# Kernel optimization log

Measured on AMD Instinct MI355X. Metric: run time of the kernel, lower is better.

Reference implementation:

```python
import jax, jax.numpy as jnp
import numpy as np

NUM_HEADS = 12
C_HEAD_DIM = 4   # int(1/dim_ratio)
S_HEAD_DIM = 16  # head_dim * dim_ratio
HEAD_DIM = C_HEAD_DIM * S_HEAD_DIM  # 64


def setup_inputs() -> dict:
    key = jax.random.key(0)
    ks = jax.random.split(key, 5)
    B, N, C, D = 8, 196, 12, 768
    x = jax.random.normal(ks[0], (B, N, C, D), dtype=jnp.float32)
    w_qkv_c = jax.random.normal(ks[1], (NUM_HEADS * 3 * C_HEAD_DIM, D), dtype=jnp.float32) * 0.02
    w_qkv_s = jax.random.normal(ks[2], (NUM_HEADS * 3 * S_HEAD_DIM, D), dtype=jnp.float32) * 0.02
    w_proj = jax.random.normal(ks[3], (D, D), dtype=jnp.float32) * 0.02
    b_proj = jnp.zeros((D,), dtype=jnp.float32)
    return {"x": x, "w_qkv_c": w_qkv_c, "w_qkv_s": w_qkv_s, "w_proj": w_proj, "b_proj": b_proj}


def _sdpa(q, k, v):
    # PyTorch F.scaled_dot_product_attention default scale: 1/sqrt(q.shape[-1])
    scale = q.shape[-1] ** -0.5
    attn = jax.nn.softmax(jnp.einsum('...qd,...kd->...qk', q * scale, k), axis=-1)
    return jnp.einsum('...qk,...kd->...qd', attn, v)


def reference(x, w_qkv_c, w_qkv_s, w_proj, b_proj):
    B, N, C, D = x.shape
    H, chd, shd = NUM_HEADS, C_HEAD_DIM, S_HEAD_DIM
    # channel-attention qkv: (3, B, H, N, C, chd)
    qkv_c = (x @ w_qkv_c.T).reshape(B, N, C, 3, H, chd).transpose(3, 0, 4, 1, 2, 5)
    qc, kc, vc = qkv_c[0], qkv_c[1], qkv_c[2]
    # spatial-attention qkv: (3, B, H, N, C, shd) -> attend over N
    qkv_s = (x @ w_qkv_s.T).reshape(B, N, C, 3, H, shd).transpose(3, 0, 4, 1, 2, 5)
    qs, ks, vs = qkv_s[0], qkv_s[1], qkv_s[2]
    qs, ks, vs = (t.swapaxes(-2, -3) for t in (qs, ks, vs))  # (B,H,C,N,shd)
    # spatial attention over N, then back to (B,H,N,C,shd)
    xs = _sdpa(qs, ks, vs).swapaxes(-2, -3)
    # channel attention over C: (B,H,N,C,chd)
    xc = _sdpa(qc, kc, vc)
    # outer product combine: (B,H,N,C,chd,shd) -> (B,H,N,C,head_dim)
    out = (xc[..., :, None] * xs[..., None, :]).reshape(B, H, N, C, chd * shd)
    # (B,N,H,C,hd) -> reshape (B,N,C,D) (row-major, matches torch)
    out = out.swapaxes(1, 2).reshape(B, N, C, D)
    return out @ w_proj.T + b_proj
```

## Files before the change

### kernel.cpp

```cpp
#include <hip/hip_runtime.h>
#include <math.h>

#define B_  8
#define N_  196
#define C_  12
#define D_  768
#define H_  12
#define R_  (B_*N_*C_)
#define KDIM 768
#define NQKV_PAD 768

typedef _Float16 f16x8 __attribute__((ext_vector_type(8)));
typedef _Float16 f16x4 __attribute__((ext_vector_type(4)));
typedef __fp16 fp16x2 __attribute__((ext_vector_type(2)));
typedef __attribute__((ext_vector_type(4))) float f32x4;

__device__ inline unsigned short f2h(float f) {
    union { _Float16 h; unsigned short u; } v; v.h = (_Float16)f; return v.u;
}
__device__ inline float h2f(unsigned short u) {
    union { unsigned short u; _Float16 h; } v; v.u = u; return (float)v.h;
}
__device__ inline unsigned pk2u(float a, float b) {
    union { fp16x2 h; unsigned u; } v;
    v.h = __builtin_amdgcn_cvt_pkrtz(a, b);
    return v.u;
}
__device__ inline unsigned scale2(unsigned u, float s) {
    return pk2u(h2f((unsigned short)(u & 0xffff)) * s,
                h2f((unsigned short)(u >> 16)) * s);
}

__global__ __launch_bounds__(256) void convert_weights(
    const float* __restrict__ wc, const float* __restrict__ ws,
    const float* __restrict__ wp,
    unsigned short* __restrict__ wqkv_h, unsigned short* __restrict__ wp_h)
{
    int i = (blockIdx.x * 256 + threadIdx.x) * 4;
    float4 v; unsigned short* dh; int off;
    if (i < 768 * 768) {
        off = i;
        const int r = off / 768, k = off % 768;
        v = make_float4(0.f, 0.f, 0.f, 0.f);
        if (r < 144)      v = *reinterpret_cast<const float4*>(wc + r * 768 + k);
        else if (r < 720) v = *reinterpret_cast<const float4*>(ws + (r - 144) * 768 + k);
        dh = wqkv_h;
    } else {
        off = i - 768 * 768;
        if (off >= 768 * 768) return;
        v = *reinterpret_cast<const float4*>(wp + off);
        dh = wp_h;
    }
    uint2 h;
    h.x = pk2u(v.x, v.y);
    h.y = pk2u(v.z, v.w);
    *reinterpret_cast<uint2*>(dh + off) = h;
}

#define BM 128
#define BN 128
#define BK 64

__device__ inline void gload16(const unsigned short* src, void* ldsbase) {
    __builtin_amdgcn_global_load_lds(
        (const __attribute__((address_space(1))) unsigned int*)src,
        (__attribute__((address_space(3))) unsigned int*)ldsbase, 16, 0, 0);
}

__global__ __launch_bounds__(512, 2) void gemm_qkv_fused(
    const float* __restrict__ Af, const unsigned short* __restrict__ Bh,
    unsigned short* __restrict__ outh, int M, int Nt, int K, int ntiles)
{
    __shared__ unsigned short sA[2][BM][BK];
    __shared__ unsigned short sB[2][BN][BK];

    const int nwg = gridDim.x;
    const int bid = blockIdx.x;
    const int xcd = bid & 7, slot = bid >> 3;
    const int q = nwg >> 3, r = nwg & 7;
    const int wg = (xcd < r ? xcd * (q + 1) : r * (q + 1) + (xcd - r) * q) + slot;
    const int mt = wg / ntiles, nt = wg - mt * ntiles;
    const int m0 = mt * BM, n0 = nt * BN;

    const int tid = threadIdx.x;
    const int w = tid >> 6, l = tid & 63;
    const int fl = l & 15, g = l >> 4;
    const int wr = (w >> 2) * 64;
    const int wc = (w & 3) * 32;

    f32x4 acc[4][2];
    #pragma unroll
    for (int i = 0; i < 4; ++i)
        #pragma unroll
        for (int j = 0; j < 2; ++j)
            acc[i][j] = (f32x4){0.f, 0.f, 0.f, 0.f};

    const int srow = w * 16 + (l >> 3);
    const int scol = ((l & 7) ^ (l >> 3)) * 8;

    float4 a0, a1, a2, a3;

#define LOADA(kk) {                                                                         \
    const float* paf = Af + (size_t)(m0 + srow) * K + (kk) + scol;                          \
    a0 = *reinterpret_cast<const float4*>(paf);                                             \
    a1 = *reinterpret_cast<const float4*>(paf + 4);                                         \
    a2 = *reinterpret_cast<const float4*>(paf + 8 * K);                                     \
    a3 = *reinterpret_cast<const float4*>(paf + 8 * K + 4); }

#define WRITEA(buf) {                                                                       \
    char* da = (char*)sA + (buf) * 16384 + w * 2048 + l * 16;                               \
    uint4 v0 = { pk2u(a0.x,a0.y), pk2u(a0.z,a0.w), pk2u(a1.x,a1.y), pk2u(a1.z,a1.w) };      \
    uint4 v1 = { pk2u(a2.x,a2.y), pk2u(a2.z,a2.w), pk2u(a3.x,a3.y), pk2u(a3.z,a3.w) };      \
    *reinterpret_cast<uint4*>(da) = v0;                                                     \
    *reinterpret_cast<uint4*>(da + 1024) = v1; }

#define STAGEB(buf, kk) {                                                                   \
    const unsigned short* pb = Bh + (size_t)(n0 + srow) * K + (kk) + scol;                  \
    char* db = (char*)sB + (buf) * 16384 + w * 2048;                                        \
    gload16(pb,          db);                                                               \
    gload16(pb + 8 * K,  db + 1024); }

    LOADA(0);
    STAGEB(0, 0);
    asm volatile("s_waitcnt vmcnt(2)" ::: "memory");
    WRITEA(0);
    LOADA(BK);
    asm volatile("s_waitcnt lgkmcnt(0)" ::: "memory");

    const int KT = K / BK;
    int cur = 0;
    for (int t = 0; t < KT; ++t) {
        if (t + 1 < KT) {
            STAGEB(cur ^ 1, (t + 1) * BK);
            asm volatile("s_waitcnt vmcnt(2)" ::: "memory");
        } else {
            asm volatile("s_waitcnt vmcnt(0)" ::: "memory");
        }
        asm volatile("s_barrier" ::: "memory");

        {
            const int rcol = (g ^ (fl & 7)) * 8;
            f16x8 ah[4];
            #pragma unroll
            for (int fm = 0; fm < 4; ++fm)
                ah[fm] = *reinterpret_cast<const f16x8*>(&sA[cur][wr + fm * 16 + fl][rcol]);
            __builtin_amdgcn_s_setprio(1);
            #pragma unroll
            for (int fn = 0; fn < 2; ++fn) {
                const f16x8 bf = *reinterpret_cast<const f16x8*>(&sB[cur][wc + fn * 16 + fl][rcol]);
                #pragma unroll
                for (int fm = 0; fm < 4; ++fm)
                    acc[fm][fn] = __builtin_amdgcn_mfma_f32_16x16x32_f16(ah[fm], bf, acc[fm][fn], 0, 0, 0);
            }
            __builtin_amdgcn_s_setprio(0);
        }
        if (t + 1 < KT) WRITEA(cur ^ 1);
        if (t + 2 < KT) LOADA((t + 2) * BK);
        {
            const int rcol = ((4 + g) ^ (fl & 7)) * 8;
            f16x8 ah[4];
            #pragma unroll
            for (int fm = 0; fm < 4; ++fm)
                ah[fm] = *reinterpret_cast<const f16x8*>(&sA[cur][wr + fm * 16 + fl][rcol]);
            __builtin_amdgcn_s_setprio(1);
            #pragma unroll
            for (int fn = 0; fn < 2; ++fn) {
                const f16x8 bf = *reinterpret_cast<const f16x8*>(&sB[cur][wc + fn * 16 + fl][rcol]);
                #pragma unroll
                for (int fm = 0; fm < 4; ++fm)
                    acc[fm][fn] = __builtin_amdgcn_mfma_f32_16x16x32_f16(ah[fm], bf, acc[fm][fn], 0, 0, 0);
            }
            __builtin_amdgcn_s_setprio(0);
        }
        asm volatile("s_waitcnt lgkmcnt(0)" ::: "memory");
        asm volatile("s_barrier" ::: "memory");
        cur ^= 1;
    }
#undef LOADA
#undef WRITEA
#undef STAGEB

    const int rg = g * 4;
    #pragma unroll
    for (int fm = 0; fm < 4; ++fm)
        #pragma unroll
        for (int fn = 0; fn < 2; ++fn) {
            const int row = m0 + wr + fm * 16 + rg;
            const int col = n0 + wc + fn * 16 + fl;
            #pragma unroll
            for (int rr = 0; rr < 4; ++rr)
                outh[(size_t)(row + rr) * Nt + col] = f2h(acc[fm][fn][rr]);
        }
}

__global__ __launch_bounds__(512, 2) void gemm_f16(
    const unsigned short* __restrict__ Ah, const unsigned short* __restrict__ Bh,
    const float* __restrict__ bias,
    float* __restrict__ outp, int M, int Nt, int K, int ntiles)
{
    __shared__ unsigned short sA[2][BM][BK];
    __shared__ unsigned short sB[2][BN][BK];

    const int nwg = gridDim.x;
    const int bid = blockIdx.x;
    const int xcd = bid & 7, slot = bid >> 3;
    const int q = nwg >> 3, r = nwg & 7;
    const int wg = (xcd < r ? xcd * (q + 1) : r * (q + 1) + (xcd - r) * q) + slot;
    const int mt = wg / ntiles, nt = wg - mt * ntiles;
    const int m0 = mt * BM, n0 = nt * BN;

    const int tid = threadIdx.x;
    const int w = tid >> 6, l = tid & 63;
    const int fl = l & 15, g = l >> 4;
    const int wr = (w >> 2) * 64;
    const int wc = (w & 3) * 32;

    f32x4 acc[4][2];
    #pragma unroll
    for (int i = 0; i < 4; ++i)
        #pragma unroll
        for (int j = 0; j < 2; ++j)
            acc[i][j] = (f32x4){0.f, 0.f, 0.f, 0.f};

    const int srow = w * 16 + (l >> 3);
    const int scol = ((l & 7) ^ (l >> 3)) * 8;

#define STAGE(buf, kk) {                                                                    \
    const unsigned short* pa = Ah + (size_t)(m0 + srow) * K + (kk) + scol;                  \
    const unsigned short* pb = Bh + (size_t)(n0 + srow) * K + (kk) + scol;                  \
    char* da = (char*)sA + (buf) * 16384 + w * 2048;                                        \
    char* db = (char*)sB + (buf) * 16384 + w * 2048;                                        \
    gload16(pa,          da);                                                               \
    gload16(pa + 8 * K,  da + 1024);                                                        \
    gload16(pb,          db);                                                               \
    gload16(pb + 8 * K,  db + 1024); }

    STAGE(0, 0);

    const int KT = K / BK;
    int cur = 0;
    for (int t = 0; t < KT; ++t) {
        if (t + 1 < KT) {
            STAGE(cur ^ 1, (t + 1) * BK);
            asm volatile("s_waitcnt vmcnt(4)" ::: "memory");
        } else {
            asm volatile("s_waitcnt vmcnt(0)" ::: "memory");
        }
        asm volatile("s_barrier" ::: "memory");

        #pragma unroll
        for (int ks = 0; ks < 2; ++ks) {
            const int rcol = ((ks * 4 + g) ^ (fl & 7)) * 8;
            f16x8 ah[4];
            #pragma unroll
            for (int fm = 0; fm < 4; ++fm)
                ah[fm] = *reinterpret_cast<const f16x8*>(&sA[cur][wr + fm * 16 + fl][rcol]);
            __builtin_amdgcn_s_setprio(1);
            #pragma unroll
            for (int fn = 0; fn < 2; ++fn) {
                const f16x8 bf = *reinterpret_cast<const f16x8*>(&sB[cur][wc + fn * 16 + fl][rcol]);
                #pragma unroll
                for (int fm = 0; fm < 4; ++fm)
                    acc[fm][fn] = __builtin_amdgcn_mfma_f32_16x16x32_f16(ah[fm], bf, acc[fm][fn], 0, 0, 0);
            }
            __builtin_amdgcn_s_setprio(0);
        }
        asm volatile("s_barrier" ::: "memory");
        cur ^= 1;
    }
#undef STAGE

    const int rg = g * 4;
    #pragma unroll
    for (int fm = 0; fm < 4; ++fm)
        #pragma unroll
        for (int fn = 0; fn < 2; ++fn) {
            const int row = m0 + wr + fm * 16 + rg;
            const int col = n0 + wc + fn * 16 + fl;
            const float bv = bias[col];
            #pragma unroll
            for (int rr = 0; rr < 4; ++rr)
                outp[(size_t)(row + rr) * Nt + col] = acc[fm][fn][rr] + bv;
        }
}

__global__ __launch_bounds__(256) void spatial_attn_mfma(
    const unsigned short* __restrict__ qkv,
    unsigned short* __restrict__ xs_out)
{
    __shared__ unsigned short Kl[224][24];
    __shared__ unsigned short Ql[208][24];
    __shared__ unsigned short Vt[16][236];

    const int bid2 = blockIdx.x;
    const int half = bid2 & 1;
    const int bid = bid2 >> 1;
    const int c = bid % 12;
    const int h = (bid / 12) % 12;
    const int b = bid / 144;
    const int tid = threadIdx.x;
    const int w = tid >> 6, l = tid & 63;
    const int fl = l & 15, g = l >> 4;
    const int qbase = half * 7;
    const int ntl = 7 - half;

    const float qs = 0.25f * 1.4426950408889634f;
    for (int idx = tid; idx < N_ * 2; idx += 256) {
        const int n = idx >> 1, eh = (idx & 1) * 8;
        const unsigned short* base =
            qkv + (size_t)((b * N_ + n) * 12 + c) * NQKV_PAD + 144 + h * 16 + eh;
        const uint4 q4 = *reinterpret_cast<const uint4*>(base);
        const uint4 k4 = *reinterpret_cast<const uint4*>(base + 192);
        const uint4 v4 = *reinterpret_cast<const uint4*>(base + 384);
        uint4 qsc;
        qsc.x = scale2(q4.x, qs); qsc.y = scale2(q4.y, qs);
        qsc.z = scale2(q4.z, qs); qsc.w = scale2(q4.w, qs);
        *reinterpret_cast<uint4*>(&Ql[n][eh]) = qsc;
        *reinterpret_cast<uint4*>(&Kl[n][eh]) = k4;
        Vt[eh + 0][n] = (unsigned short)(v4.x & 0xffff);
        Vt[eh + 1][n] = (unsigned short)(v4.x >> 16);
        Vt[eh + 2][n] = (unsigned short)(v4.y & 0xffff);
        Vt[eh + 3][n] = (unsigned short)(v4.y >> 16);
        Vt[eh + 4][n] = (unsigned short)(v4.z & 0xffff);
        Vt[eh + 5][n] = (unsigned short)(v4.z >> 16);
        Vt[eh + 6][n] = (unsigned short)(v4.w & 0xffff);
        Vt[eh + 7][n] = (unsigned short)(v4.w >> 16);
    }
    for (int idx = tid; idx < 16 * 28; idx += 256) {
        const int d = idx / 28, n = 196 + idx % 28;
        Vt[d][n] = 0;
    }
    __syncthreads();

    f32x4 accO[2];
    float lsum[2];
    #pragma unroll
    for (int j = 0; j < 2; ++j) {
        accO[j] = (f32x4){0.f, 0.f, 0.f, 0.f};
        lsum[j] = 0.f;
    }
    const f32x4 zf = (f32x4){0.f, 0.f, 0.f, 0.f};

    f16x4 Bq[2];
    #pragma unroll
    for (int j = 0; j < 2; ++j) {
        const int qtl = w + 4 * j;
        const int qt = (qtl < ntl) ? (qbase + qtl) : 12;
        Bq[j] = *reinterpret_cast<const f16x4*>(&Ql[qt * 16 + fl][4 * g]);
    }

    for (int ch = 0; ch < 7; ++ch) {
        const int kb0 = ch * 32;
        const f16x4 Ak0 = *reinterpret_cast<const f16x4*>(&Kl[kb0 + fl][4 * g]);
        const f16x4 Ak1 = *reinterpret_cast<const f16x4*>(&Kl[kb0 + 16 + fl][4 * g]);
        const f16x4 Av0 = *reinterpret_cast<const f16x4*>(&Vt[fl][kb0 + 4 * g]);
        const f16x4 Av1 = *reinterpret_cast<const f16x4*>(&Vt[fl][kb0 + 16 + 4 * g]);

        #pragma unroll
        for (int j = 0; j < 2; ++j) {
            if (w + 4 * j >= ntl) continue;

            __builtin_amdgcn_s_setprio(1);
            f32x4 T0 = __builtin_amdgcn_mfma_f32_16x16x16f16(Ak0, Bq[j], zf, 0, 0, 0);
            f32x4 T1 = __builtin_amdgcn_mfma_f32_16x16x16f16(Ak1, Bq[j], zf, 0, 0, 0);
            __builtin_amdgcn_s_setprio(0);

            float s0 = T0[0], s1 = T0[1], s2 = T0[2], s3 = T0[3];
            float s4 = T1[0], s5 = T1[1], s6 = T1[2], s7 = T1[3];
            if (ch == 6) {
                const int kg = kb0 + 4 * g;
                if (kg + 0 >= 196) s0 = -1e30f;
                if (kg + 1 >= 196) s1 = -1e30f;
                if (kg + 2 >= 196) s2 = -1e30f;
                if (kg + 3 >= 196) s3 = -1e30f;
                s4 = -1e30f; s5 = -1e30f; s6 = -1e30f; s7 = -1e30f;
            }
            const float p0 = exp2f(s0), p1 = exp2f(s1);
            const float p2 = exp2f(s2), p3 = exp2f(s3);
            const float p4 = exp2f(s4), p5 = exp2f(s5);
            const float p6 = exp2f(s6), p7 = exp2f(s7);
            lsum[j] += ((p0 + p1) + (p2 + p3)) + ((p4 + p5) + (p6 + p7));

            union { unsigned u[2]; f16x4 v; } pa, pb;
            pa.u[0] = pk2u(p0, p1); pa.u[1] = pk2u(p2, p3);
            pb.u[0] = pk2u(p4, p5); pb.u[1] = pk2u(p6, p7);

            __builtin_amdgcn_s_setprio(1);
            accO[j] = __builtin_amdgcn_mfma_f32_16x16x16f16(Av0, pa.v, accO[j], 0, 0, 0);
            accO[j] = __builtin_amdgcn_mfma_f32_16x16x16f16(Av1, pb.v, accO[j], 0, 0, 0);
            __builtin_amdgcn_s_setprio(0);
        }
    }

    #pragma unroll
    for (int j = 0; j < 2; ++j) {
        const int qtl = w + 4 * j;
        if (qtl >= ntl) continue;
        const int qt = qbase + qtl;
        float ls = lsum[j];
        ls += __shfl_xor(ls, 16);
        ls += __shfl_xor(ls, 32);
        const int n = qt * 16 + fl;
        if (n < 196) {
            const float inv = 1.f / ls;
            uint2 o;
            o.x = pk2u(accO[j][0] * inv, accO[j][1] * inv);
            o.y = pk2u(accO[j][2] * inv, accO[j][3] * inv);
            const size_t base = ((size_t)((b * 12 + h) * N_ + n) * 12 + c) * 16 + 4 * g;
            *reinterpret_cast<uint2*>(&xs_out[base]) = o;
        }
    }
}

__global__ __launch_bounds__(256) void chan_attn_combine4(
    const unsigned short* __restrict__ qkv,
    const unsigned short* __restrict__ xs,
    unsigned short* __restrict__ yh)
{
    const int sub = threadIdx.x >> 6;
    const int t = threadIdx.x & 63;
    const int flat = blockIdx.x * 4 + sub;
    const int n = flat % 196;
    const int h = (flat / 196) % 12;
    const int b = flat / 2352;

    __shared__ float sQ[4][12][4], sK[4][12][4], sV[4][12][4], sXc[4][12][4];
    __shared__ float sXs[4][12][16];

    if (t < 36) {
        const int cc = t / 3, s = t % 3;
        const unsigned short* p =
            qkv + (size_t)((b * N_ + n) * 12 + cc) * NQKV_PAD + s * 48 + h * 4;
        const ushort4 v4 = *reinterpret_cast<const ushort4*>(p);
        float* dst = (s == 0) ? &sQ[sub][cc][0] : (s == 1) ? &sK[sub][cc][0] : &sV[sub][cc][0];
        dst[0] = h2f(v4.x); dst[1] = h2f(v4.y); dst[2] = h2f(v4.z); dst[3] = h2f(v4.w);
    }
    if (t < 48) {
        const int cc = t >> 2, j0 = (t & 3) * 4;
        const ushort4 v4 =
            *reinterpret_cast<const ushort4*>(&xs[((size_t)flat * 12 + cc) * 16 + j0]);
        sXs[sub][cc][j0 + 0] = h2f(v4.x);
        sXs[sub][cc][j0 + 1] = h2f(v4.y);
        sXs[sub][cc][j0 + 2] = h2f(v4.z);
        sXs[sub][cc][j0 + 3] = h2f(v4.w);
    }
    __syncthreads();

    if (t < 12) {
        const int c = t;
        float s[12];
        float m = -INFINITY;
        #pragma unroll
        for (int c2 = 0; c2 < 12; ++c2) {
            float d = 0.f;
            #pragma unroll
            for (int e = 0; e < 4; ++e) d += sQ[sub][c][e] * sK[sub][c2][e];
            s[c2] = d * 0.5f;
            m = fmaxf(m, s[c2]);
        }
        float lsum = 0.f;
        #pragma unroll
        for (int c2 = 0; c2 < 12; ++c2) { s[c2] = __expf(s[c2] - m); lsum += s[c2]; }
        const float inv = 1.f / lsum;
        #pragma unroll
        for (int i = 0; i < 4; ++i) {
            float a = 0.f;
            #pragma unroll
            for (int c2 = 0; c2 < 12; ++c2) a += s[c2] * sV[sub][c2][i];
            sXc[sub][c][i] = a * inv;
        }
    }
    __syncthreads();

    const size_t yrow = ((size_t)(b * N_ + n) * 12 + h) * (size_t)D_;
    #pragma unroll
    for (int k = 0; k < 12; ++k) {
        const float v = sXc[sub][k][t >> 4] * sXs[sub][k][t & 15];
        yh[yrow + k * 64 + t] = f2h(v);
    }
}

extern "C" void kernel_launch(void* const* d_in, const int* in_sizes, int n_in,
                              void* d_out, int out_size, void* d_ws, size_t ws_size,
                              hipStream_t stream) {
    const float* x       = (const float*)d_in[0];
    const float* w_qkv_c = (const float*)d_in[1];
    const float* w_qkv_s = (const float*)d_in[2];
    const float* w_proj  = (const float*)d_in[3];
    const float* b_proj  = (const float*)d_in[4];
    float* out = (float*)d_out;

    unsigned short* yh     = (unsigned short*)d_ws;
    unsigned short* wqkv_h = yh + (size_t)R_ * KDIM;
    unsigned short* wp_h   = wqkv_h + (size_t)768 * 768;
    unsigned short* qkv_h  = wp_h + (size_t)768 * 768;
    unsigned short* xs_h   = qkv_h + (size_t)R_ * NQKV_PAD;

    {
        const int total = (2 * 768 * 768) / 4;
        convert_weights<<<(total + 255) / 256, 256, 0, stream>>>(
            w_qkv_c, w_qkv_s, w_proj, wqkv_h, wp_h);
    }
    {
        const int mtiles = R_ / BM, ntiles = NQKV_PAD / BN;
        gemm_qkv_fused<<<mtiles * ntiles, 512, 0, stream>>>(
            x, wqkv_h, qkv_h, R_, NQKV_PAD, KDIM, ntiles);
    }
    spatial_attn_mfma<<<B_ * H_ * C_ * 2, 256, 0, stream>>>(qkv_h, xs_h);
    chan_attn_combine4<<<(B_ * H_ * N_) / 4, 256, 0, stream>>>(qkv_h, xs_h, yh);
    {
        const int mtiles = R_ / BM, ntiles = D_ / BN;
        gemm_f16<<<mtiles * ntiles, 512, 0, stream>>>(
            yh, wp_h, b_proj, out, R_, D_, KDIM, ntiles);
    }
}
```

Before: 122.1 us.

## Compute channel attention first and fuse outer-product combine into spatial attention epilogue

```diff
diff --git a/kernel.cpp b/kernel.cpp
--- a/kernel.cpp
+++ b/kernel.cpp
@@ -284,9 +284,64 @@
         }
 }
 
+__global__ __launch_bounds__(256) void chan_attn_xc(
+    const unsigned short* __restrict__ qkv,
+    unsigned short* __restrict__ xc)
+{
+    const int sub = threadIdx.x >> 6;
+    const int t = threadIdx.x & 63;
+    const int flat = blockIdx.x * 4 + sub;
+    const int n = flat % 196;
+    const int h = (flat / 196) % 12;
+    const int b = flat / 2352;
+
+    __shared__ float sQ[4][12][4], sK[4][12][4], sV[4][12][4];
+
+    if (t < 36) {
+        const int cc = t / 3, s = t % 3;
+        const unsigned short* p =
+            qkv + (size_t)((b * N_ + n) * 12 + cc) * NQKV_PAD + s * 48 + h * 4;
+        const ushort4 v4 = *reinterpret_cast<const ushort4*>(p);
+        float* dst = (s == 0) ? &sQ[sub][cc][0] : (s == 1) ? &sK[sub][cc][0] : &sV[sub][cc][0];
+        dst[0] = h2f(v4.x); dst[1] = h2f(v4.y); dst[2] = h2f(v4.z); dst[3] = h2f(v4.w);
+    }
+    __syncthreads();
+
+    if (t < 12) {
+        const int c = t;
+        float s[12];
+        float m = -INFINITY;
+        #pragma unroll
+        for (int c2 = 0; c2 < 12; ++c2) {
+            float d = 0.f;
+            #pragma unroll
+            for (int e = 0; e < 4; ++e) d += sQ[sub][c][e] * sK[sub][c2][e];
+            s[c2] = d * 0.5f;
+            m = fmaxf(m, s[c2]);
+        }
+        float lsum = 0.f;
+        #pragma unroll
+        for (int c2 = 0; c2 < 12; ++c2) { s[c2] = __expf(s[c2] - m); lsum += s[c2]; }
+        const float inv = 1.f / lsum;
+        float xcv[4];
+        #pragma unroll
+        for (int i = 0; i < 4; ++i) {
+            float a = 0.f;
+            #pragma unroll
+            for (int c2 = 0; c2 < 12; ++c2) a += s[c2] * sV[sub][c2][i];
+            xcv[i] = a * inv;
+        }
+        uint2 o;
+        o.x = pk2u(xcv[0], xcv[1]);
+        o.y = pk2u(xcv[2], xcv[3]);
+        *reinterpret_cast<uint2*>(xc + (size_t)flat * 48 + c * 4) = o;
+    }
+}
+
 __global__ __launch_bounds__(256) void spatial_attn_mfma(
     const unsigned short* __restrict__ qkv,
-    unsigned short* __restrict__ xs_out)
+    const unsigned short* __restrict__ xc,
+    unsigned short* __restrict__ y)
 {
     __shared__ unsigned short Kl[224][24];
     __shared__ unsigned short Ql[208][24];
@@ -403,80 +458,24 @@
         const int n = qt * 16 + fl;
         if (n < 196) {
             const float inv = 1.f / ls;
+            const float o0 = accO[j][0] * inv, o1 = accO[j][1] * inv;
+            const float o2 = accO[j][2] * inv, o3 = accO[j][3] * inv;
+            const ushort4 xc4 = *reinterpret_cast<const ushort4*>(
+                xc + (size_t)((b * 12 + h) * 196 + n) * 48 + c * 4);
+            const float x0 = h2f(xc4.x), x1 = h2f(xc4.y);
+            const float x2 = h2f(xc4.z), x3 = h2f(xc4.w);
+            unsigned short* yrow =
+                y + ((size_t)(b * N_ + n) * 12 + h) * (size_t)D_ + c * 64 + 4 * g;
             uint2 o;
-            o.x = pk2u(accO[j][0] * inv, accO[j][1] * inv);
-            o.y = pk2u(accO[j][2] * inv, accO[j][3] * inv);
-            const size_t base = ((size_t)((b * 12 + h) * N_ + n) * 12 + c) * 16 + 4 * g;
-            *reinterpret_cast<uint2*>(&xs_out[base]) = o;
-        }
-    }
-}
-
-__global__ __launch_bounds__(256) void chan_attn_combine4(
-    const unsigned short* __restrict__ qkv,
-    const unsigned short* __restrict__ xs,
-    unsigned short* __restrict__ yh)
-{
-    const int sub = threadIdx.x >> 6;
-    const int t = threadIdx.x & 63;
-    const int flat = blockIdx.x * 4 + sub;
-    const int n = flat % 196;
-    const int h = (flat / 196) % 12;
-    const int b = flat / 2352;
-
-    __shared__ float sQ[4][12][4], sK[4][12][4], sV[4][12][4], sXc[4][12][4];
-    __shared__ float sXs[4][12][16];
-
-    if (t < 36) {
-        const int cc = t / 3, s = t % 3;
-        const unsigned short* p =
-            qkv + (size_t)((b * N_ + n) * 12 + cc) * NQKV_PAD + s * 48 + h * 4;
-        const ushort4 v4 = *reinterpret_cast<const ushort4*>(p);
-        float* dst = (s == 0) ? &sQ[sub][cc][0] : (s == 1) ? &sK[sub][cc][0] : &sV[sub][cc][0];
-        dst[0] = h2f(v4.x); dst[1] = h2f(v4.y); dst[2] = h2f(v4.z); dst[3] = h2f(v4.w);
-    }
-    if (t < 48) {
-        const int cc = t >> 2, j0 = (t & 3) * 4;
-        const ushort4 v4 =
-            *reinterpret_cast<const ushort4*>(&xs[((size_t)flat * 12 + cc) * 16 + j0]);
-        sXs[sub][cc][j0 + 0] = h2f(v4.x);
-        sXs[sub][cc][j0 + 1] = h2f(v4.y);
-        sXs[sub][cc][j0 + 2] = h2f(v4.z);
-        sXs[sub][cc][j0 + 3] = h2f(v4.w);
-    }
-    __syncthreads();
-
-    if (t < 12) {
-        const int c = t;
-        float s[12];
-        float m = -INFINITY;
-        #pragma unroll
-        for (int c2 = 0; c2 < 12; ++c2) {
-            float d = 0.f;
-            #pragma unroll
-            for (int e = 0; e < 4; ++e) d += sQ[sub][c][e] * sK[sub][c2][e];
-            s[c2] = d * 0.5f;
-            m = fmaxf(m, s[c2]);
-        }
-        float lsum = 0.f;
-        #pragma unroll
-        for (int c2 = 0; c2 < 12; ++c2) { s[c2] = __expf(s[c2] - m); lsum += s[c2]; }
-        const float inv = 1.f / lsum;
-        #pragma unroll
-        for (int i = 0; i < 4; ++i) {
-            float a = 0.f;
-            #pragma unroll
-            for (int c2 = 0; c2 < 12; ++c2) a += s[c2] * sV[sub][c2][i];
-            sXc[sub][c][i] = a * inv;
-        }
-    }
-    __syncthreads();
-
-    const size_t yrow = ((size_t)(b * N_ + n) * 12 + h) * (size_t)D_;
-    #pragma unroll
-    for (int k = 0; k < 12; ++k) {
-        const float v = sXc[sub][k][t >> 4] * sXs[sub][k][t & 15];
-        yh[yrow + k * 64 + t] = f2h(v);
+            o.x = pk2u(x0 * o0, x0 * o1); o.y = pk2u(x0 * o2, x0 * o3);
+            *reinterpret_cast<uint2*>(yrow) = o;
+            o.x = pk2u(x1 * o0, x1 * o1); o.y = pk2u(x1 * o2, x1 * o3);
+            *reinterpret_cast<uint2*>(yrow + 16) = o;
+            o.x = pk2u(x2 * o0, x2 * o1); o.y = pk2u(x2 * o2, x2 * o3);
+            *reinterpret_cast<uint2*>(yrow + 32) = o;
+            o.x = pk2u(x3 * o0, x3 * o1); o.y = pk2u(x3 * o2, x3 * o3);
+            *reinterpret_cast<uint2*>(yrow + 48) = o;
+        }
     }
 }
 
@@ -494,7 +493,7 @@
     unsigned short* wqkv_h = yh + (size_t)R_ * KDIM;
     unsigned short* wp_h   = wqkv_h + (size_t)768 * 768;
     unsigned short* qkv_h  = wp_h + (size_t)768 * 768;
-    unsigned short* xs_h   = qkv_h + (size_t)R_ * NQKV_PAD;
+    unsigned short* xc_h   = qkv_h + (size_t)R_ * NQKV_PAD;
 
     {
         const int total = (2 * 768 * 768) / 4;
@@ -506,8 +505,8 @@
         gemm_qkv_fused<<<mtiles * ntiles, 512, 0, stream>>>(
             x, wqkv_h, qkv_h, R_, NQKV_PAD, KDIM, ntiles);
     }
-    spatial_attn_mfma<<<B_ * H_ * C_ * 2, 256, 0, stream>>>(qkv_h, xs_h);
-    chan_attn_combine4<<<(B_ * H_ * N_) / 4, 256, 0, stream>>>(qkv_h, xs_h, yh);
+    chan_attn_xc<<<(B_ * H_ * N_) / 4, 256, 0, stream>>>(qkv_h, xc_h);
+    spatial_attn_mfma<<<B_ * H_ * C_ * 2, 256, 0, stream>>>(qkv_h, xc_h, yh);
     {
         const int mtiles = R_ / BM, ntiles = D_ / BN;
         gemm_f16<<<mtiles * ntiles, 512, 0, stream>>>(
```

New measurement: 120.5 us. Within noise of the previous version (-1.3%).
